# Performance work log

Measured on AMD Instinct MI355X. Metric: run time of the kernel, lower is better.

The kernel has to match this reference:

```python
import jax, jax.numpy as jnp
import numpy as np

D, H, O, NEXP, NA = 128, 256, 128, 8, 5  # na = max(1, int(8*0.7)) = 5
T = float(np.e)  # gate temperature
N_TOKENS = 131072


def ternary_quantize(w):
    # per-expert-matrix threshold: alpha = mean(|W|) over each [out,in] matrix
    alpha = jnp.mean(jnp.abs(w), axis=(-2, -1), keepdims=True)
    return jnp.sign(w) * (jnp.abs(w) > 0.5 * alpha).astype(w.dtype)


def setup_inputs() -> dict:
    key = jax.random.key(0)
    ks = jax.random.split(key, 7)
    x = jax.random.normal(ks[0], (N_TOKENS, D), dtype=jnp.float32)
    # expert params stacked over expert dim e (nn.Linear layout: [out, in])
    w1 = jax.random.normal(ks[1], (NEXP, H, D), dtype=jnp.float32) * 0.05
    b1 = jax.random.normal(ks[2], (NEXP, H), dtype=jnp.float32) * 0.05
    w2 = jax.random.normal(ks[3], (NEXP, O, H), dtype=jnp.float32) * 0.05
    b2 = jax.random.normal(ks[4], (NEXP, O), dtype=jnp.float32) * 0.05
    wg = jax.random.normal(ks[5], (NEXP, D), dtype=jnp.float32) * 0.05
    bg = jax.random.normal(ks[6], (NEXP,), dtype=jnp.float32) * 0.05
    return {"x": x, "w1": w1, "b1": b1, "w2": w2, "b2": b2, "wg": wg, "bg": bg}


def reference(x, w1, b1, w2, b2, wg, bg):
    # Ternary-quantize expert weights on the fly (TW.forward); dropout in eval mode (identity).
    w1q = ternary_quantize(w1)
    w2q = ternary_quantize(w2)
    # all-expert dense MLP: x [t,d] -> hidden [t,e,h] -> eo [t,e,o]
    hid = jax.nn.relu(jnp.einsum('td,ehd->teh', x, w1q) + b1[None, :, :])
    eo = jnp.einsum('teh,eoh->teo', hid, w2q) + b2[None, :, :]
    # BG gate: tempered softmax, top-k mask, renormalize
    p = jax.nn.softmax((x @ wg.T + bg) / T, axis=-1)          # [t,e]
    _, idx = jax.lax.top_k(p, NA)                             # [t,na]
    m = jnp.sum(jax.nn.one_hot(idx, NEXP, dtype=p.dtype), axis=-2)  # [t,e] 0/1 mask
    w = p * m
    w = w / (jnp.sum(w, axis=-1, keepdims=True) + 1e-8)
    return jnp.einsum('te,teo->to', w, eo)
```

## Files before the change

kernel.cpp:

```cpp
#include <hip/hip_runtime.h>
#include <hip/hip_bf16.h>

typedef unsigned int u32;
typedef unsigned short u16;
using f32x4  = __attribute__((ext_vector_type(4))) float;
using f32x16 = __attribute__((ext_vector_type(16))) float;
using u32x4  = __attribute__((ext_vector_type(4))) u32;
using s16x8  = __attribute__((ext_vector_type(8))) short;

#define DEV static __device__ __forceinline__

DEV u32 pk2(float a, float b) {
  u16 lo = __builtin_bit_cast(u16, __float2bfloat16(a));
  u16 hi = __builtin_bit_cast(u16, __float2bfloat16(b));
  return (u32)lo | ((u32)hi << 16);
}

DEV f32x16 MFMA32(u32x4 a, u32x4 b, f32x16 c) {
  return __builtin_amdgcn_mfma_f32_32x32x16_bf16(
      __builtin_bit_cast(s16x8, a), __builtin_bit_cast(s16x8, b), c, 0, 0, 0);
}

DEV void pl32swap(u32& a, u32& b) {
  asm volatile("v_permlane32_swap_b32 %0, %1" : "+v"(a), "+v"(b));
}

typedef const __attribute__((address_space(1))) u32 gu32;
typedef __attribute__((address_space(3))) u32 lu32;

DEV void load_lds16(const void* g, void* l) {
  __builtin_amdgcn_global_load_lds((gu32*)g, (lu32*)l, 16, 0, 0);
}

__global__ void qalpha(const float* __restrict__ w1, const float* __restrict__ w2,
                       float* __restrict__ alphas) {
  int b = blockIdx.x;
  const float* src = (b < 8 ? w1 : w2) + (size_t)(b & 7) * 32768;
  int tid = threadIdx.x;
  float s = 0.f;
  for (int i = tid; i < 32768; i += 256) s += fabsf(src[i]);
  #pragma unroll
  for (int off = 32; off >= 1; off >>= 1) s += __shfl_down(s, off, 64);
  __shared__ float ws4[4];
  if ((tid & 63) == 0) ws4[tid >> 6] = s;
  __syncthreads();
  if (tid == 0) alphas[b] = (ws4[0] + ws4[1] + ws4[2] + ws4[3]) * (1.f / 32768.f);
}

DEV u16 tq1(float v, float thr) {
  return (fabsf(v) > thr) ? (v > 0.f ? (u16)0x3F80 : (u16)0xBF80) : (u16)0;
}
DEV u32 tq2(float a, float b, float thr) {
  return (u32)tq1(a, thr) | ((u32)tq1(b, thr) << 16);
}

__global__ void qimg(const float* __restrict__ w1, const float* __restrict__ w2,
                     const float* __restrict__ alphas,
                     char* __restrict__ img1, char* __restrict__ img2) {
  int gid = blockIdx.x * 256 + threadIdx.x;
  if (gid < 32768) {
    int e = gid >> 12, rem = gid & 4095;
    int h = rem >> 4, slot = rem & 15;
    int k0 = (slot >> 1) * 16 + (slot & 1) * 8;
    const float* src = w1 + (size_t)e * 32768 + h * 128 + k0;
    float thr = 0.5f * alphas[e];
    float4 v0 = *(const float4*)src;
    float4 v1 = *(const float4*)(src + 4);
    u32 q0 = tq2(v0.x, v0.y, thr), q1 = tq2(v0.z, v0.w, thr);
    u32 q2 = tq2(v1.x, v1.y, thr), q3 = tq2(v1.z, v1.w, thr);
    int ht = h >> 5, row = h & 31;
    char* dst = img1 + ((size_t)e << 16) + ht * 8192 + row * 256 +
                (((u32)slot * 16) ^ ((u32)(row & 15) << 4));
    *(uint4*)dst = make_uint4(q0, q1, q2, q3);
  } else if (gid < 65536) {
    int id = gid - 32768;
    int e = id >> 12, rem = id & 4095;
    int c = rem >> 9, o = (rem >> 2) & 127, kslot = rem & 3;
    int k0 = c * 32 + (kslot >> 1) * 16 + (kslot & 1) * 8;
    const float* src = w2 + (size_t)e * 32768 + o * 256 + k0;
    float thr = 0.5f * alphas[8 + e];
    float4 v0 = *(const float4*)src;
    float4 v1 = *(const float4*)(src + 4);
    u32 q0 = tq2(v0.x, v0.y, thr), q1 = tq2(v0.z, v0.w, thr);
    u32 q2 = tq2(v1.x, v1.y, thr), q3 = tq2(v1.z, v1.w, thr);
    int og = o >> 2, slot = (o & 3) * 4 + kslot;
    char* dst = img2 + ((size_t)e << 16) + c * 8192 + og * 256 +
                (((u32)slot * 16) ^ ((u32)(og & 7) << 4));
    *(uint4*)dst = make_uint4(q0, q1, q2, q3);
  }
}

#define LDS_B1 32768
#define LDS_B2 40960
#define LDS_G  45056
#define SMEM_BYTES 57344

__global__ __launch_bounds__(256, 2) void moe_main(
    const float* __restrict__ x, const float* __restrict__ b1g,
    const float* __restrict__ b2g, const float* __restrict__ wg,
    const float* __restrict__ bg, const char* __restrict__ img1,
    const char* __restrict__ img2, float* __restrict__ out) {
  extern __shared__ char smem[];
  const int tid = threadIdx.x;
  const int w = tid >> 6, l = tid & 63;
  const int col = l & 31, hi = l >> 5;
  const int tokw = blockIdx.x * 256 + w * 64;

  {
    const char* s1 = img1 + w * 2048 + l * 16;
    const char* s2 = img2 + w * 2048 + l * 16;
    load_lds16(s1,        smem + w * 2048);
    load_lds16(s1 + 1024, smem + w * 2048 + 1024);
    load_lds16(s2,        smem + 8192 + w * 2048);
    load_lds16(s2 + 1024, smem + 8192 + w * 2048 + 1024);
    load_lds16((const char*)b1g + w * 2048 + l * 16, smem + LDS_B1 + w * 2048);
    load_lds16((const char*)b1g + w * 2048 + 1024 + l * 16,
               smem + LDS_B1 + w * 2048 + 1024);
    load_lds16((const char*)b2g + w * 1024 + l * 16, smem + LDS_B2 + w * 1024);
  }

  u32x4 xf[2][8];
  #pragma unroll
  for (int tt = 0; tt < 2; ++tt) {
    #pragma unroll
    for (int ks = 0; ks < 8; ++ks) {
      const float* xp = x + (size_t)(tokw + tt * 32 + col) * 128 + ks * 16 + hi * 8;
      float4 v0 = *(const float4*)xp;
      float4 v1 = *(const float4*)(xp + 4);
      xf[tt][ks] = (u32x4){pk2(v0.x, v0.y), pk2(v0.z, v0.w),
                           pk2(v1.x, v1.y), pk2(v1.z, v1.w)};
    }
  }

  {
    int t = blockIdx.x * 256 + tid;
    const float4* xr = (const float4*)(x + (size_t)t * 128);
    const float4* wr = (const float4*)wg;
    float lg[8];
    #pragma unroll
    for (int e = 0; e < 8; ++e) lg[e] = bg[e];
    for (int i = 0; i < 32; ++i) {
      float4 xv = xr[i];
      #pragma unroll
      for (int e = 0; e < 8; ++e) {
        float4 wv = wr[e * 32 + i];
        lg[e] += xv.x * wv.x + xv.y * wv.y + xv.z * wv.z + xv.w * wv.w;
      }
    }
    const float invT = 0.36787944117144233f;
    #pragma unroll
    for (int e = 0; e < 8; ++e) lg[e] *= invT;
    float mx = lg[0];
    #pragma unroll
    for (int e = 1; e < 8; ++e) mx = fmaxf(mx, lg[e]);
    float p[8], den = 0.f;
    #pragma unroll
    for (int e = 0; e < 8; ++e) { p[e] = __expf(lg[e] - mx); den += p[e]; }
    float inv = 1.f / den;
    #pragma unroll
    for (int e = 0; e < 8; ++e) p[e] *= inv;
    float gsel[8], wsum = 0.f;
    #pragma unroll
    for (int e = 0; e < 8; ++e) {
      int rank = 0;
      #pragma unroll
      for (int e2 = 0; e2 < 8; ++e2)
        rank += (p[e2] > p[e]) || (p[e2] == p[e] && e2 < e);
      gsel[e] = (rank < 5) ? p[e] : 0.f;
      wsum += gsel[e];
    }
    float r = 1.f / (wsum + 1e-8f);
    float* gr = (float*)(smem + LDS_G) + tid * 12;
    *(f32x4*)gr       = (f32x4){gsel[0] * r, gsel[1] * r, gsel[2] * r, gsel[3] * r};
    *(f32x4*)(gr + 4) = (f32x4){gsel[4] * r, gsel[5] * r, gsel[6] * r, gsel[7] * r};
  }
  __syncthreads();

  f32x16 acc2[4][2];
  {
    u32x4 gf[2];
    #pragma unroll
    for (int tt = 0; tt < 2; ++tt) {
      u32x4 v = (u32x4){0u, 0u, 0u, 0u};
      if (hi == 0) {
        const float* gr = (const float*)(smem + LDS_G) + (w * 64 + tt * 32 + col) * 12;
        f32x4 g0 = *(const f32x4*)gr;
        f32x4 g1 = *(const f32x4*)(gr + 4);
        v = (u32x4){pk2(g0.x, g0.y), pk2(g0.z, g0.w), pk2(g1.x, g1.y), pk2(g1.z, g1.w)};
      }
      gf[tt] = v;
    }
    const float* b2r = (const float*)(smem + LDS_B2);
    #pragma unroll
    for (int ot = 0; ot < 4; ++ot) {
      u32x4 af = (u32x4){0u, 0u, 0u, 0u};
      if (hi == 0) {
        int o = ot * 32 + col;
        af = (u32x4){pk2(b2r[0 * 128 + o], b2r[1 * 128 + o]),
                     pk2(b2r[2 * 128 + o], b2r[3 * 128 + o]),
                     pk2(b2r[4 * 128 + o], b2r[5 * 128 + o]),
                     pk2(b2r[6 * 128 + o], b2r[7 * 128 + o])};
      }
      f32x16 z{};
      #pragma unroll
      for (int tt = 0; tt < 2; ++tt) acc2[ot][tt] = MFMA32(af, gf[tt], z);
    }
  }

  const u32 rb1 = (u32)(col * 256);
  int cur = 0;
  for (int n = 0; n < 64; ++n) {
    const int e = n >> 3, ht = n & 7;
    if (n + 1 < 64) {
      const int n1 = n + 1, e1 = n1 >> 3, ht1 = n1 & 7;
      const char* s1 = img1 + ((size_t)e1 << 16) + ht1 * 8192 + w * 2048 + l * 16;
      const char* s2 = img2 + ((size_t)e1 << 16) + ht1 * 8192 + w * 2048 + l * 16;
      char* d1 = smem + (cur ^ 1) * 16384 + w * 2048;
      char* d2 = smem + (cur ^ 1) * 16384 + 8192 + w * 2048;
      load_lds16(s1,        d1);
      load_lds16(s1 + 1024, d1 + 1024);
      load_lds16(s2,        d2);
      load_lds16(s2 + 1024, d2 + 1024);
    }

    const char* w1c = smem + cur * 16384;
    f32x16 a1_0{}, a1_1{};
    #pragma unroll
    for (int ks = 0; ks < 8; ++ks) {
      u32 off = rb1 + (((u32)(ks * 2 + hi) * 16) ^ ((u32)(l & 15) << 4));
      u32x4 frag = *(const u32x4*)(w1c + off);
      a1_0 = MFMA32(frag, xf[0][ks], a1_0);
      a1_1 = MFMA32(frag, xf[1][ks], a1_1);
    }

    u32x4 hf[2][2];
    const float* b1b = (const float*)(smem + LDS_B1) + e * 256 + ht * 32 + hi * 4;
    #pragma unroll
    for (int tt = 0; tt < 2; ++tt) {
      const f32x16& a1 = tt ? a1_1 : a1_0;
      float g = ((const float*)(smem + LDS_G))[(w * 64 + tt * 32 + col) * 12 + e];
      u32 u[8];
      #pragma unroll
      for (int rg = 0; rg < 4; ++rg) {
        f32x4 bb = *(const f32x4*)(b1b + rg * 8);
        float h0 = fmaxf(a1[rg * 4 + 0] + bb.x, 0.f) * g;
        float h1 = fmaxf(a1[rg * 4 + 1] + bb.y, 0.f) * g;
        float h2 = fmaxf(a1[rg * 4 + 2] + bb.z, 0.f) * g;
        float h3 = fmaxf(a1[rg * 4 + 3] + bb.w, 0.f) * g;
        u[rg * 2 + 0] = pk2(h0, h1);
        u[rg * 2 + 1] = pk2(h2, h3);
      }
      pl32swap(u[0], u[2]);
      pl32swap(u[1], u[3]);
      pl32swap(u[4], u[6]);
      pl32swap(u[5], u[7]);
      hf[0][tt] = (u32x4){u[0], u[1], u[2], u[3]};
      hf[1][tt] = (u32x4){u[4], u[5], u[6], u[7]};
    }

    const char* w2c = smem + cur * 16384 + 8192;
    #pragma unroll
    for (int ks2 = 0; ks2 < 2; ++ks2) {
      #pragma unroll
      for (int ot = 0; ot < 4; ++ot) {
        u32 og = (u32)(ot * 8 + (col >> 2));
        u32 slot = (u32)((col & 3) * 4 + ks2 * 2 + hi);
        u32 off = og * 256 + ((slot * 16) ^ ((og & 7) << 4));
        u32x4 af = *(const u32x4*)(w2c + off);
        acc2[ot][0] = MFMA32(af, hf[ks2][0], acc2[ot][0]);
        acc2[ot][1] = MFMA32(af, hf[ks2][1], acc2[ot][1]);
      }
    }
    __syncthreads();
    cur ^= 1;
  }

  #pragma unroll
  for (int ot = 0; ot < 4; ++ot) {
    #pragma unroll
    for (int tt = 0; tt < 2; ++tt) {
      const f32x16& a = acc2[ot][tt];
      float* op = out + (size_t)(tokw + tt * 32 + col) * 128 + ot * 32 + hi * 4;
      #pragma unroll
      for (int rg = 0; rg < 4; ++rg)
        *(f32x4*)(op + rg * 8) =
            (f32x4){a[rg * 4 + 0], a[rg * 4 + 1], a[rg * 4 + 2], a[rg * 4 + 3]};
    }
  }
}

extern "C" void kernel_launch(void* const* d_in, const int* in_sizes, int n_in,
                              void* d_out, int out_size, void* d_ws, size_t ws_size,
                              hipStream_t stream) {
  const float* x  = (const float*)d_in[0];
  const float* w1 = (const float*)d_in[1];
  const float* b1 = (const float*)d_in[2];
  const float* w2 = (const float*)d_in[3];
  const float* b2 = (const float*)d_in[4];
  const float* wg = (const float*)d_in[5];
  const float* bg = (const float*)d_in[6];
  float* out = (float*)d_out;

  if (ws_size < 1048640) return;
  char* ws = (char*)d_ws;
  char* img1 = ws;
  char* img2 = ws + 524288;
  float* alphas = (float*)(ws + 1048576);

  int ntok = in_sizes[0] / 128;
  int nblk = ntok / 256;

  qalpha<<<16, 256, 0, stream>>>(w1, w2, alphas);
  qimg<<<256, 256, 0, stream>>>(w1, w2, alphas, img1, img2);

  hipFuncSetAttribute(reinterpret_cast<const void*>(moe_main),
                      hipFuncAttributeMaxDynamicSharedMemorySize, SMEM_BYTES);
  moe_main<<<nblk, 256, SMEM_BYTES, stream>>>(x, b1, b2, wg, bg, img1, img2, out);
}
```

Before: 188.7 us.

## Triple-buffer expert weight tiles with explicit vmcnt waits and one barrier per step

Expands the LDS weight ring from two to three stages and prefetches two steps ahead. A partial vmcnt wait plus a raw s_barrier replaces the full __syncthreads at the end of each iteration. The gate table is transposed to an expert-major layout, so per-expert gate values are hoisted out of the inner loop. MFMA sections are wrapped in s_setprio. This raises LDS use per block, which may cut the number of blocks resident per CU, and the hand-written waitcnt logic depends on the exact count of outstanding loads.

Result: no change. 187.2 us (-0.8%).

```diff
diff --git a/kernel.cpp b/kernel.cpp
--- a/kernel.cpp
+++ b/kernel.cpp
@@ -90,10 +90,10 @@
   }
 }
 
-#define LDS_B1 32768
-#define LDS_B2 40960
-#define LDS_G  45056
-#define SMEM_BYTES 57344
+#define LDS_B1 49152
+#define LDS_B2 57344
+#define LDS_G  61440
+#define SMEM_BYTES 69632
 
 __global__ __launch_bounds__(256, 2) void moe_main(
     const float* __restrict__ x, const float* __restrict__ b1g,
@@ -113,6 +113,10 @@
     load_lds16(s1 + 1024, smem + w * 2048 + 1024);
     load_lds16(s2,        smem + 8192 + w * 2048);
     load_lds16(s2 + 1024, smem + 8192 + w * 2048 + 1024);
+    load_lds16(s1 + 8192,        smem + 16384 + w * 2048);
+    load_lds16(s1 + 8192 + 1024, smem + 16384 + w * 2048 + 1024);
+    load_lds16(s2 + 8192,        smem + 16384 + 8192 + w * 2048);
+    load_lds16(s2 + 8192 + 1024, smem + 16384 + 8192 + w * 2048 + 1024);
     load_lds16((const char*)b1g + w * 2048 + l * 16, smem + LDS_B1 + w * 2048);
     load_lds16((const char*)b1g + w * 2048 + 1024 + l * 16,
                smem + LDS_B1 + w * 2048 + 1024);
@@ -170,23 +174,25 @@
       wsum += gsel[e];
     }
     float r = 1.f / (wsum + 1e-8f);
-    float* gr = (float*)(smem + LDS_G) + tid * 12;
-    *(f32x4*)gr       = (f32x4){gsel[0] * r, gsel[1] * r, gsel[2] * r, gsel[3] * r};
-    *(f32x4*)(gr + 4) = (f32x4){gsel[4] * r, gsel[5] * r, gsel[6] * r, gsel[7] * r};
+    float* gT = (float*)(smem + LDS_G);
+    #pragma unroll
+    for (int e = 0; e < 8; ++e) gT[e * 256 + tid] = gsel[e] * r;
   }
   __syncthreads();
 
   f32x16 acc2[4][2];
   {
+    const float* gT = (const float*)(smem + LDS_G);
     u32x4 gf[2];
     #pragma unroll
     for (int tt = 0; tt < 2; ++tt) {
       u32x4 v = (u32x4){0u, 0u, 0u, 0u};
       if (hi == 0) {
-        const float* gr = (const float*)(smem + LDS_G) + (w * 64 + tt * 32 + col) * 12;
-        f32x4 g0 = *(const f32x4*)gr;
-        f32x4 g1 = *(const f32x4*)(gr + 4);
-        v = (u32x4){pk2(g0.x, g0.y), pk2(g0.z, g0.w), pk2(g1.x, g1.y), pk2(g1.z, g1.w)};
+        int t = w * 64 + tt * 32 + col;
+        v = (u32x4){pk2(gT[0 * 256 + t], gT[1 * 256 + t]),
+                    pk2(gT[2 * 256 + t], gT[3 * 256 + t]),
+                    pk2(gT[4 * 256 + t], gT[5 * 256 + t]),
+                    pk2(gT[6 * 256 + t], gT[7 * 256 + t])};
       }
       gf[tt] = v;
     }
@@ -208,71 +214,95 @@
   }
 
   const u32 rb1 = (u32)(col * 256);
-  int cur = 0;
-  for (int n = 0; n < 64; ++n) {
-    const int e = n >> 3, ht = n & 7;
-    if (n + 1 < 64) {
-      const int n1 = n + 1, e1 = n1 >> 3, ht1 = n1 & 7;
-      const char* s1 = img1 + ((size_t)e1 << 16) + ht1 * 8192 + w * 2048 + l * 16;
-      const char* s2 = img2 + ((size_t)e1 << 16) + ht1 * 8192 + w * 2048 + l * 16;
-      char* d1 = smem + (cur ^ 1) * 16384 + w * 2048;
-      char* d2 = smem + (cur ^ 1) * 16384 + 8192 + w * 2048;
-      load_lds16(s1,        d1);
-      load_lds16(s1 + 1024, d1 + 1024);
-      load_lds16(s2,        d2);
-      load_lds16(s2 + 1024, d2 + 1024);
-    }
-
-    const char* w1c = smem + cur * 16384;
-    f32x16 a1_0{}, a1_1{};
-    #pragma unroll
-    for (int ks = 0; ks < 8; ++ks) {
-      u32 off = rb1 + (((u32)(ks * 2 + hi) * 16) ^ ((u32)(l & 15) << 4));
-      u32x4 frag = *(const u32x4*)(w1c + off);
-      a1_0 = MFMA32(frag, xf[0][ks], a1_0);
-      a1_1 = MFMA32(frag, xf[1][ks], a1_1);
-    }
-
-    u32x4 hf[2][2];
-    const float* b1b = (const float*)(smem + LDS_B1) + e * 256 + ht * 32 + hi * 4;
-    #pragma unroll
-    for (int tt = 0; tt < 2; ++tt) {
-      const f32x16& a1 = tt ? a1_1 : a1_0;
-      float g = ((const float*)(smem + LDS_G))[(w * 64 + tt * 32 + col) * 12 + e];
-      u32 u[8];
-      #pragma unroll
-      for (int rg = 0; rg < 4; ++rg) {
-        f32x4 bb = *(const f32x4*)(b1b + rg * 8);
-        float h0 = fmaxf(a1[rg * 4 + 0] + bb.x, 0.f) * g;
-        float h1 = fmaxf(a1[rg * 4 + 1] + bb.y, 0.f) * g;
-        float h2 = fmaxf(a1[rg * 4 + 2] + bb.z, 0.f) * g;
-        float h3 = fmaxf(a1[rg * 4 + 3] + bb.w, 0.f) * g;
-        u[rg * 2 + 0] = pk2(h0, h1);
-        u[rg * 2 + 1] = pk2(h2, h3);
-      }
-      pl32swap(u[0], u[2]);
-      pl32swap(u[1], u[3]);
-      pl32swap(u[4], u[6]);
-      pl32swap(u[5], u[7]);
-      hf[0][tt] = (u32x4){u[0], u[1], u[2], u[3]};
-      hf[1][tt] = (u32x4){u[4], u[5], u[6], u[7]};
-    }
-
-    const char* w2c = smem + cur * 16384 + 8192;
-    #pragma unroll
-    for (int ks2 = 0; ks2 < 2; ++ks2) {
-      #pragma unroll
-      for (int ot = 0; ot < 4; ++ot) {
-        u32 og = (u32)(ot * 8 + (col >> 2));
-        u32 slot = (u32)((col & 3) * 4 + ks2 * 2 + hi);
-        u32 off = og * 256 + ((slot * 16) ^ ((og & 7) << 4));
-        u32x4 af = *(const u32x4*)(w2c + off);
-        acc2[ot][0] = MFMA32(af, hf[ks2][0], acc2[ot][0]);
-        acc2[ot][1] = MFMA32(af, hf[ks2][1], acc2[ot][1]);
-      }
-    }
-    __syncthreads();
-    cur ^= 1;
+  const u32 x1 = (u32)((l & 15) << 4);
+  const char* sp1 = img1 + 16384 + w * 2048 + l * 16;
+  const char* sp2 = img2 + 16384 + w * 2048 + l * 16;
+  int cur = 0, wr = 2;
+
+  #pragma unroll 1
+  for (int e = 0; e < 8; ++e) {
+    const float* gTe = (const float*)(smem + LDS_G) + e * 256 + w * 64 + col;
+    const float g0 = gTe[0];
+    const float g1 = gTe[32];
+    const float* b1e = (const float*)(smem + LDS_B1) + e * 256 + hi * 4;
+
+    #pragma unroll 1
+    for (int ht = 0; ht < 8; ++ht) {
+      const int n = e * 8 + ht;
+      if (n > 0) {
+        if (n < 63) asm volatile("s_waitcnt vmcnt(4)" ::: "memory");
+        else        asm volatile("s_waitcnt vmcnt(0)" ::: "memory");
+        __builtin_amdgcn_s_barrier();
+        asm volatile("" ::: "memory");
+        __builtin_amdgcn_sched_barrier(0);
+      }
+
+      if (n + 2 < 64) {
+        char* d1 = smem + wr * 16384 + w * 2048;
+        char* d2 = d1 + 8192;
+        load_lds16(sp1,        d1);
+        load_lds16(sp1 + 1024, d1 + 1024);
+        load_lds16(sp2,        d2);
+        load_lds16(sp2 + 1024, d2 + 1024);
+      }
+      sp1 += 8192; sp2 += 8192;
+
+      const char* w1c = smem + cur * 16384;
+      f32x16 a1_0{}, a1_1{};
+      __builtin_amdgcn_s_setprio(1);
+      #pragma unroll
+      for (int ks = 0; ks < 8; ++ks) {
+        u32 off = rb1 + (((u32)((ks * 2 + hi) * 16)) ^ x1);
+        u32x4 frag = *(const u32x4*)(w1c + off);
+        a1_0 = MFMA32(frag, xf[0][ks], a1_0);
+        a1_1 = MFMA32(frag, xf[1][ks], a1_1);
+      }
+      __builtin_amdgcn_s_setprio(0);
+
+      u32x4 hf[2][2];
+      const float* b1b = b1e + ht * 32;
+      #pragma unroll
+      for (int tt = 0; tt < 2; ++tt) {
+        const f32x16& a1 = tt ? a1_1 : a1_0;
+        const float g = tt ? g1 : g0;
+        u32 u[8];
+        #pragma unroll
+        for (int rg = 0; rg < 4; ++rg) {
+          f32x4 bb = *(const f32x4*)(b1b + rg * 8);
+          float h0 = fmaxf(a1[rg * 4 + 0] + bb.x, 0.f) * g;
+          float h1 = fmaxf(a1[rg * 4 + 1] + bb.y, 0.f) * g;
+          float h2 = fmaxf(a1[rg * 4 + 2] + bb.z, 0.f) * g;
+          float h3 = fmaxf(a1[rg * 4 + 3] + bb.w, 0.f) * g;
+          u[rg * 2 + 0] = pk2(h0, h1);
+          u[rg * 2 + 1] = pk2(h2, h3);
+        }
+        pl32swap(u[0], u[2]);
+        pl32swap(u[1], u[3]);
+        pl32swap(u[4], u[6]);
+        pl32swap(u[5], u[7]);
+        hf[0][tt] = (u32x4){u[0], u[1], u[2], u[3]};
+        hf[1][tt] = (u32x4){u[4], u[5], u[6], u[7]};
+      }
+
+      const char* w2c = w1c + 8192;
+      __builtin_amdgcn_s_setprio(1);
+      #pragma unroll
+      for (int ks2 = 0; ks2 < 2; ++ks2) {
+        #pragma unroll
+        for (int ot = 0; ot < 4; ++ot) {
+          u32 og = (u32)(ot * 8 + (col >> 2));
+          u32 slot = (u32)((col & 3) * 4 + ks2 * 2 + hi);
+          u32 off = og * 256 + ((slot * 16) ^ ((og & 7) << 4));
+          u32x4 af = *(const u32x4*)(w2c + off);
+          acc2[ot][0] = MFMA32(af, hf[ks2][0], acc2[ot][0]);
+          acc2[ot][1] = MFMA32(af, hf[ks2][1], acc2[ot][1]);
+        }
+      }
+      __builtin_amdgcn_s_setprio(0);
+
+      cur = (cur == 2) ? 0 : cur + 1;
+      wr  = (wr  == 2) ? 0 : wr  + 1;
+    }
   }
 
   #pragma unroll
```

## Load pre-swizzled MFMA weight fragments directly from global into registers, drop LDS staging

Applied to the files above, without the earlier changes.

The quantization kernel now writes weights in exact per-lane MFMA fragment order, so the main kernel loads each fragment straight from global/L2 into registers instead of double-buffering tiles through LDS with global_load_lds. This removes the per-step __syncthreads and LDS reads and shrinks shared memory, which could raise occupancy. It also adds s_setprio around the MFMA bursts and moves gate weights to a transposed LDS layout. The risk is that weight loads now go to L2 every step with no prefetch, which can expose memory latency.

Measured after the change: 346.8 us. 83.7% more time.

```diff
diff --git a/kernel.cpp b/kernel.cpp
--- a/kernel.cpp
+++ b/kernel.cpp
@@ -23,13 +23,6 @@
 
 DEV void pl32swap(u32& a, u32& b) {
   asm volatile("v_permlane32_swap_b32 %0, %1" : "+v"(a), "+v"(b));
-}
-
-typedef const __attribute__((address_space(1))) u32 gu32;
-typedef __attribute__((address_space(3))) u32 lu32;
-
-DEV void load_lds16(const void* g, void* l) {
-  __builtin_amdgcn_global_load_lds((gu32*)g, (lu32*)l, 16, 0, 0);
 }
 
 __global__ void qalpha(const float* __restrict__ w1, const float* __restrict__ w2,
@@ -55,68 +48,58 @@
 }
 
 __global__ void qimg(const float* __restrict__ w1, const float* __restrict__ w2,
-                     const float* __restrict__ alphas,
-                     char* __restrict__ img1, char* __restrict__ img2) {
+                     const float* __restrict__ alphas, char* __restrict__ img) {
   int gid = blockIdx.x * 256 + threadIdx.x;
+  int l = gid & 63;
+  int col = l & 31, hi = l >> 5;
+  const float* src;
+  float thr;
+  char* dst;
   if (gid < 32768) {
-    int e = gid >> 12, rem = gid & 4095;
-    int h = rem >> 4, slot = rem & 15;
-    int k0 = (slot >> 1) * 16 + (slot & 1) * 8;
-    const float* src = w1 + (size_t)e * 32768 + h * 128 + k0;
-    float thr = 0.5f * alphas[e];
-    float4 v0 = *(const float4*)src;
-    float4 v1 = *(const float4*)(src + 4);
-    u32 q0 = tq2(v0.x, v0.y, thr), q1 = tq2(v0.z, v0.w, thr);
-    u32 q2 = tq2(v1.x, v1.y, thr), q3 = tq2(v1.z, v1.w, thr);
-    int ht = h >> 5, row = h & 31;
-    char* dst = img1 + ((size_t)e << 16) + ht * 8192 + row * 256 +
-                (((u32)slot * 16) ^ ((u32)(row & 15) << 4));
-    *(uint4*)dst = make_uint4(q0, q1, q2, q3);
-  } else if (gid < 65536) {
+    int ks = (gid >> 6) & 7;
+    int n  = gid >> 9;
+    int e  = n >> 3, ht = n & 7;
+    int h  = ht * 32 + col;
+    int k0 = ks * 16 + hi * 8;
+    src = w1 + (size_t)e * 32768 + h * 128 + k0;
+    thr = 0.5f * alphas[e];
+    dst = img + (size_t)n * 16384 + ks * 1024 + l * 16;
+  } else {
     int id = gid - 32768;
-    int e = id >> 12, rem = id & 4095;
-    int c = rem >> 9, o = (rem >> 2) & 127, kslot = rem & 3;
-    int k0 = c * 32 + (kslot >> 1) * 16 + (kslot & 1) * 8;
-    const float* src = w2 + (size_t)e * 32768 + o * 256 + k0;
-    float thr = 0.5f * alphas[8 + e];
-    float4 v0 = *(const float4*)src;
-    float4 v1 = *(const float4*)(src + 4);
-    u32 q0 = tq2(v0.x, v0.y, thr), q1 = tq2(v0.z, v0.w, thr);
-    u32 q2 = tq2(v1.x, v1.y, thr), q3 = tq2(v1.z, v1.w, thr);
-    int og = o >> 2, slot = (o & 3) * 4 + kslot;
-    char* dst = img2 + ((size_t)e << 16) + c * 8192 + og * 256 +
-                (((u32)slot * 16) ^ ((u32)(og & 7) << 4));
-    *(uint4*)dst = make_uint4(q0, q1, q2, q3);
-  }
-}
-
-#define LDS_B1 32768
-#define LDS_B2 40960
-#define LDS_G  45056
-#define SMEM_BYTES 57344
+    int sl = (id >> 6) & 7;
+    int n  = id >> 9;
+    int e  = n >> 3, c = n & 7;
+    int ks2 = sl >> 2, ot = sl & 3;
+    int o  = ot * 32 + col;
+    int k0 = c * 32 + ks2 * 16 + hi * 8;
+    src = w2 + (size_t)e * 32768 + o * 256 + k0;
+    thr = 0.5f * alphas[8 + e];
+    dst = img + (size_t)n * 16384 + 8192 + sl * 1024 + l * 16;
+  }
+  float4 v0 = *(const float4*)src;
+  float4 v1 = *(const float4*)(src + 4);
+  u32 q0 = tq2(v0.x, v0.y, thr), q1 = tq2(v0.z, v0.w, thr);
+  u32 q2 = tq2(v1.x, v1.y, thr), q3 = tq2(v1.z, v1.w, thr);
+  *(uint4*)dst = make_uint4(q0, q1, q2, q3);
+}
 
 __global__ __launch_bounds__(256, 2) void moe_main(
     const float* __restrict__ x, const float* __restrict__ b1g,
     const float* __restrict__ b2g, const float* __restrict__ wg,
-    const float* __restrict__ bg, const char* __restrict__ img1,
-    const char* __restrict__ img2, float* __restrict__ out) {
-  extern __shared__ char smem[];
+    const float* __restrict__ bg, const char* __restrict__ img,
+    float* __restrict__ out) {
+  __shared__ float s_b1[2048];
+  __shared__ float s_g[8 * 256];
   const int tid = threadIdx.x;
   const int w = tid >> 6, l = tid & 63;
   const int col = l & 31, hi = l >> 5;
   const int tokw = blockIdx.x * 256 + w * 64;
 
   {
-    const char* s1 = img1 + w * 2048 + l * 16;
-    const char* s2 = img2 + w * 2048 + l * 16;
-    load_lds16(s1,        smem + w * 2048);
-    load_lds16(s1 + 1024, smem + w * 2048 + 1024);
-    load_lds16(s2,        smem + 8192 + w * 2048);
-    load_lds16(s2 + 1024, smem + 8192 + w * 2048 + 1024);
-    load_lds16((const char*)b1g + w * 2048 + l * 16, smem + LDS_B1 + w * 2048);
-    load_lds16((const char*)b1g + w * 2048 + 1024 + l * 16,
-               smem + LDS_B1 + w * 2048 + 1024);
-    load_lds16((const char*)b2g + w * 1024 + l * 16, smem + LDS_B2 + w * 1024);
+    const float4* s = (const float4*)b1g;
+    float4* d = (float4*)s_b1;
+    d[tid] = s[tid];
+    d[tid + 256] = s[tid + 256];
   }
 
   u32x4 xf[2][8];
@@ -170,9 +153,8 @@
       wsum += gsel[e];
     }
     float r = 1.f / (wsum + 1e-8f);
-    float* gr = (float*)(smem + LDS_G) + tid * 12;
-    *(f32x4*)gr       = (f32x4){gsel[0] * r, gsel[1] * r, gsel[2] * r, gsel[3] * r};
-    *(f32x4*)(gr + 4) = (f32x4){gsel[4] * r, gsel[5] * r, gsel[6] * r, gsel[7] * r};
+    #pragma unroll
+    for (int e = 0; e < 8; ++e) s_g[e * 256 + tid] = gsel[e] * r;
   }
   __syncthreads();
 
@@ -183,23 +165,23 @@
     for (int tt = 0; tt < 2; ++tt) {
       u32x4 v = (u32x4){0u, 0u, 0u, 0u};
       if (hi == 0) {
-        const float* gr = (const float*)(smem + LDS_G) + (w * 64 + tt * 32 + col) * 12;
-        f32x4 g0 = *(const f32x4*)gr;
-        f32x4 g1 = *(const f32x4*)(gr + 4);
-        v = (u32x4){pk2(g0.x, g0.y), pk2(g0.z, g0.w), pk2(g1.x, g1.y), pk2(g1.z, g1.w)};
+        int t = w * 64 + tt * 32 + col;
+        v = (u32x4){pk2(s_g[0 * 256 + t], s_g[1 * 256 + t]),
+                    pk2(s_g[2 * 256 + t], s_g[3 * 256 + t]),
+                    pk2(s_g[4 * 256 + t], s_g[5 * 256 + t]),
+                    pk2(s_g[6 * 256 + t], s_g[7 * 256 + t])};
       }
       gf[tt] = v;
     }
-    const float* b2r = (const float*)(smem + LDS_B2);
     #pragma unroll
     for (int ot = 0; ot < 4; ++ot) {
       u32x4 af = (u32x4){0u, 0u, 0u, 0u};
       if (hi == 0) {
         int o = ot * 32 + col;
-        af = (u32x4){pk2(b2r[0 * 128 + o], b2r[1 * 128 + o]),
-                     pk2(b2r[2 * 128 + o], b2r[3 * 128 + o]),
-                     pk2(b2r[4 * 128 + o], b2r[5 * 128 + o]),
-                     pk2(b2r[6 * 128 + o], b2r[7 * 128 + o])};
+        af = (u32x4){pk2(b2g[0 * 128 + o], b2g[1 * 128 + o]),
+                     pk2(b2g[2 * 128 + o], b2g[3 * 128 + o]),
+                     pk2(b2g[4 * 128 + o], b2g[5 * 128 + o]),
+                     pk2(b2g[6 * 128 + o], b2g[7 * 128 + o])};
       }
       f32x16 z{};
       #pragma unroll
@@ -207,72 +189,73 @@
     }
   }
 
-  const u32 rb1 = (u32)(col * 256);
-  int cur = 0;
-  for (int n = 0; n < 64; ++n) {
-    const int e = n >> 3, ht = n & 7;
-    if (n + 1 < 64) {
-      const int n1 = n + 1, e1 = n1 >> 3, ht1 = n1 & 7;
-      const char* s1 = img1 + ((size_t)e1 << 16) + ht1 * 8192 + w * 2048 + l * 16;
-      const char* s2 = img2 + ((size_t)e1 << 16) + ht1 * 8192 + w * 2048 + l * 16;
-      char* d1 = smem + (cur ^ 1) * 16384 + w * 2048;
-      char* d2 = smem + (cur ^ 1) * 16384 + 8192 + w * 2048;
-      load_lds16(s1,        d1);
-      load_lds16(s1 + 1024, d1 + 1024);
-      load_lds16(s2,        d2);
-      load_lds16(s2 + 1024, d2 + 1024);
-    }
-
-    const char* w1c = smem + cur * 16384;
-    f32x16 a1_0{}, a1_1{};
-    #pragma unroll
-    for (int ks = 0; ks < 8; ++ks) {
-      u32 off = rb1 + (((u32)(ks * 2 + hi) * 16) ^ ((u32)(l & 15) << 4));
-      u32x4 frag = *(const u32x4*)(w1c + off);
-      a1_0 = MFMA32(frag, xf[0][ks], a1_0);
-      a1_1 = MFMA32(frag, xf[1][ks], a1_1);
-    }
-
-    u32x4 hf[2][2];
-    const float* b1b = (const float*)(smem + LDS_B1) + e * 256 + ht * 32 + hi * 4;
-    #pragma unroll
-    for (int tt = 0; tt < 2; ++tt) {
-      const f32x16& a1 = tt ? a1_1 : a1_0;
-      float g = ((const float*)(smem + LDS_G))[(w * 64 + tt * 32 + col) * 12 + e];
-      u32 u[8];
-      #pragma unroll
-      for (int rg = 0; rg < 4; ++rg) {
-        f32x4 bb = *(const f32x4*)(b1b + rg * 8);
-        float h0 = fmaxf(a1[rg * 4 + 0] + bb.x, 0.f) * g;
-        float h1 = fmaxf(a1[rg * 4 + 1] + bb.y, 0.f) * g;
-        float h2 = fmaxf(a1[rg * 4 + 2] + bb.z, 0.f) * g;
-        float h3 = fmaxf(a1[rg * 4 + 3] + bb.w, 0.f) * g;
-        u[rg * 2 + 0] = pk2(h0, h1);
-        u[rg * 2 + 1] = pk2(h2, h3);
-      }
-      pl32swap(u[0], u[2]);
-      pl32swap(u[1], u[3]);
-      pl32swap(u[4], u[6]);
-      pl32swap(u[5], u[7]);
-      hf[0][tt] = (u32x4){u[0], u[1], u[2], u[3]};
-      hf[1][tt] = (u32x4){u[4], u[5], u[6], u[7]};
-    }
-
-    const char* w2c = smem + cur * 16384 + 8192;
-    #pragma unroll
-    for (int ks2 = 0; ks2 < 2; ++ks2) {
-      #pragma unroll
-      for (int ot = 0; ot < 4; ++ot) {
-        u32 og = (u32)(ot * 8 + (col >> 2));
-        u32 slot = (u32)((col & 3) * 4 + ks2 * 2 + hi);
-        u32 off = og * 256 + ((slot * 16) ^ ((og & 7) << 4));
-        u32x4 af = *(const u32x4*)(w2c + off);
-        acc2[ot][0] = MFMA32(af, hf[ks2][0], acc2[ot][0]);
-        acc2[ot][1] = MFMA32(af, hf[ks2][1], acc2[ot][1]);
-      }
-    }
-    __syncthreads();
-    cur ^= 1;
+  const u32 loff = (u32)(l * 16);
+  const char* wp = img;
+
+  #pragma unroll 1
+  for (int e = 0; e < 8; ++e) {
+    const float g0 = s_g[e * 256 + w * 64 + col];
+    const float g1 = s_g[e * 256 + w * 64 + 32 + col];
+    const float* b1e = s_b1 + e * 256 + hi * 4;
+
+    #pragma unroll 1
+    for (int ht = 0; ht < 8; ++ht) {
+      u32x4 f1[8], f2[8];
+      #pragma unroll
+      for (int ks = 0; ks < 8; ++ks)
+        f1[ks] = *(const u32x4*)(wp + ks * 1024 + loff);
+      #pragma unroll
+      for (int sl = 0; sl < 8; ++sl)
+        f2[sl] = *(const u32x4*)(wp + 8192 + sl * 1024 + loff);
+
+      f32x16 a1_0{}, a1_1{};
+      __builtin_amdgcn_s_setprio(1);
+      #pragma unroll
+      for (int ks = 0; ks < 8; ++ks) {
+        a1_0 = MFMA32(f1[ks], xf[0][ks], a1_0);
+        a1_1 = MFMA32(f1[ks], xf[1][ks], a1_1);
+      }
+      __builtin_amdgcn_s_setprio(0);
+
+      u32x4 hf[2][2];
+      const float* b1b = b1e + ht * 32;
+      #pragma unroll
+      for (int tt = 0; tt < 2; ++tt) {
+        const f32x16& a1 = tt ? a1_1 : a1_0;
+        const float g = tt ? g1 : g0;
+        u32 u[8];
+        #pragma unroll
+        for (int rg = 0; rg < 4; ++rg) {
+          f32x4 bb = *(const f32x4*)(b1b + rg * 8);
+          float h0 = fmaxf(a1[rg * 4 + 0] + bb.x, 0.f) * g;
+          float h1 = fmaxf(a1[rg * 4 + 1] + bb.y, 0.f) * g;
+          float h2 = fmaxf(a1[rg * 4 + 2] + bb.z, 0.f) * g;
+          float h3 = fmaxf(a1[rg * 4 + 3] + bb.w, 0.f) * g;
+          u[rg * 2 + 0] = pk2(h0, h1);
+          u[rg * 2 + 1] = pk2(h2, h3);
+        }
+        pl32swap(u[0], u[2]);
+        pl32swap(u[1], u[3]);
+        pl32swap(u[4], u[6]);
+        pl32swap(u[5], u[7]);
+        hf[0][tt] = (u32x4){u[0], u[1], u[2], u[3]};
+        hf[1][tt] = (u32x4){u[4], u[5], u[6], u[7]};
+      }
+
+      __builtin_amdgcn_s_setprio(1);
+      #pragma unroll
+      for (int ks2 = 0; ks2 < 2; ++ks2) {
+        #pragma unroll
+        for (int ot = 0; ot < 4; ++ot) {
+          u32x4 af = f2[ks2 * 4 + ot];
+          acc2[ot][0] = MFMA32(af, hf[ks2][0], acc2[ot][0]);
+          acc2[ot][1] = MFMA32(af, hf[ks2][1], acc2[ot][1]);
+        }
+      }
+      __builtin_amdgcn_s_setprio(0);
+
+      wp += 16384;
+    }
   }
 
   #pragma unroll
@@ -301,19 +284,15 @@
   const float* bg = (const float*)d_in[6];
   float* out = (float*)d_out;
 
-  if (ws_size < 1048640) return;
+  if (ws_size < 1048704) return;
   char* ws = (char*)d_ws;
-  char* img1 = ws;
-  char* img2 = ws + 524288;
+  char* img = ws;
   float* alphas = (float*)(ws + 1048576);
 
   int ntok = in_sizes[0] / 128;
   int nblk = ntok / 256;
 
   qalpha<<<16, 256, 0, stream>>>(w1, w2, alphas);
-  qimg<<<256, 256, 0, stream>>>(w1, w2, alphas, img1, img2);
-
-  hipFuncSetAttribute(reinterpret_cast<const void*>(moe_main),
-                      hipFuncAttributeMaxDynamicSharedMemorySize, SMEM_BYTES);
-  moe_main<<<nblk, 256, SMEM_BYTES, stream>>>(x, b1, b2, wg, bg, img1, img2, out);
-}
+  qimg<<<256, 256, 0, stream>>>(w1, w2, alphas, img);
+  moe_main<<<nblk, 256, 0, stream>>>(x, b1, b2, wg, bg, img, out);
+}
```
